# Kernel tuning notes

Measured on AMD Instinct MI355X. Metric: run time of the kernel, lower is better.

Reference implementation:

```python
import jax, jax.numpy as jnp
import numpy as np

N = 50000      # nodes
E = 800000     # edges
IN_C = 128
HID = 96
OUT_C = 40
L = 8          # num_layers
ALPHA = 0.1
THETA = 0.5
DROPOUT = 0.5


def setup_inputs() -> dict:
    key = jax.random.key(0)
    ks = jax.random.split(key, 6)
    x = jax.random.normal(ks[0], (N, IN_C), dtype=jnp.float32)
    edge_index = jax.random.randint(ks[1], (2, E), 0, N, dtype=jnp.int64)
    proj_w = jax.random.normal(ks[2], (IN_C, HID), dtype=jnp.float32) / np.sqrt(IN_C)
    proj_b = jnp.zeros((HID,), dtype=jnp.float32)
    conv_ws = jax.random.normal(ks[3], (L, HID, HID), dtype=jnp.float32) / np.sqrt(HID)
    out_w = jax.random.normal(ks[4], (2 * HID, OUT_C), dtype=jnp.float32) / np.sqrt(2 * HID)
    out_b = jnp.zeros((OUT_C,), dtype=jnp.float32)
    return {"x": x, "edge_index": edge_index, "proj_w": proj_w, "proj_b": proj_b,
            "conv_ws": conv_ws, "out_w": out_w, "out_b": out_b}


def reference(x, edge_index, proj_w, proj_b, conv_ws, out_w, out_b):
    # --- GCN normalization with self loops (computed once, as GCN2Conv caches it) ---
    loops = jnp.arange(N, dtype=edge_index.dtype)
    src = jnp.concatenate([edge_index[0], loops])   # [E+N]
    dst = jnp.concatenate([edge_index[1], loops])
    deg = jax.ops.segment_sum(jnp.ones(E + N, dtype=x.dtype), dst, num_segments=N)
    dis = jax.lax.rsqrt(deg)                        # deg >= 1 due to self loops
    norm = dis[src] * dis[dst]                      # [E+N]

    h0 = x @ proj_w + proj_b                        # [N, HID]
    h = h0
    key = jax.random.key(42)
    for k in range(L):
        delta = 1.0 / 2 ** k
        kq, ke, kd, key = jax.random.split(key, 4)
        # dithered quantization
        b = (jax.random.uniform(kq, h.shape, dtype=h.dtype) - 0.5) * delta
        h_q = jnp.floor((h + b) / delta) * delta - b
        # GCN2Conv: propagate + initial residual + identity mapping (shared weights)
        agg = jax.ops.segment_sum(h_q[src] * norm[:, None], dst, num_segments=N)
        t = (1.0 - ALPHA) * agg + ALPHA * h0
        beta = float(np.log(THETA / (k + 1) + 1.0))
        h = (1.0 - beta) * t + beta * (t @ conv_ws[k])
        # gaussian noise + relu
        h = jax.nn.relu(h + 0.01 * jax.random.normal(ke, h.shape, dtype=h.dtype))
        if k != L - 1:
            keep = 1.0 - DROPOUT
            mask = jax.random.bernoulli(kd, keep, h.shape)
            h = jnp.where(mask, h / keep, 0.0)
    return jnp.concatenate([h0, h], axis=-1) @ out_w + out_b
```

## Files before the change

kernel.cpp:

```cpp
#include <hip/hip_runtime.h>
#include <hip/hip_fp16.h>
#include <cstdint>
#include <cmath>

#define HID 96
#define INC 128
#define OUTC 40
#define ROWS 32

__device__ __forceinline__ unsigned rotl32d(unsigned x, int r){ return (x<<r)|(x>>(32-r)); }

__device__ __forceinline__ void tf2x32_dev(unsigned k0, unsigned k1, unsigned x0, unsigned x1,
                                           unsigned &y0, unsigned &y1){
  unsigned ks2 = k0 ^ k1 ^ 0x1BD11BDAu;
  x0 += k0; x1 += k1;
#define TFR(r) { x0 += x1; x1 = rotl32d(x1, r); x1 ^= x0; }
  TFR(13) TFR(15) TFR(26) TFR(6)   x0 += k1;  x1 += ks2 + 1u;
  TFR(17) TFR(29) TFR(16) TFR(24)  x0 += ks2; x1 += k0 + 2u;
  TFR(13) TFR(15) TFR(26) TFR(6)   x0 += k0;  x1 += k1 + 3u;
  TFR(17) TFR(29) TFR(16) TFR(24)  x0 += k1;  x1 += ks2 + 4u;
  TFR(13) TFR(15) TFR(26) TFR(6)   x0 += ks2; x1 += k0 + 5u;
#undef TFR
  y0 = x0; y1 = x1;
}

__device__ __forceinline__ unsigned tf_bits(unsigned k0, unsigned k1, unsigned idx){
  unsigned y0, y1; tf2x32_dev(k0, k1, 0u, idx, y0, y1); return y0 ^ y1;
}

__device__ __forceinline__ float u01_from_bits(unsigned bits){
  return __uint_as_float((bits >> 9) | 0x3f800000u) - 1.0f;
}

__device__ __forceinline__ float erfinv_xla(float x){
  float w = -log1pf(-x*x);
  float p;
  if (w < 5.0f){
    w = w - 2.5f;
    p = 2.81022636e-08f;
    p = fmaf(p,w, 3.43273939e-07f);
    p = fmaf(p,w,-3.5233877e-06f);
    p = fmaf(p,w,-4.39150654e-06f);
    p = fmaf(p,w, 0.00021858087f);
    p = fmaf(p,w,-0.00125372503f);
    p = fmaf(p,w,-0.00417768164f);
    p = fmaf(p,w, 0.246640727f);
    p = fmaf(p,w, 1.50140941f);
  } else {
    w = sqrtf(w) - 3.0f;
    p = -0.000200214257f;
    p = fmaf(p,w, 0.000100950558f);
    p = fmaf(p,w, 0.00134934322f);
    p = fmaf(p,w,-0.00367342844f);
    p = fmaf(p,w, 0.00573950773f);
    p = fmaf(p,w,-0.0076224613f);
    p = fmaf(p,w, 0.00943887047f);
    p = fmaf(p,w, 1.00167406f);
    p = fmaf(p,w, 2.83297682f);
  }
  return p*x;
}

__global__ void k_detect(const unsigned* __restrict__ raw, int* flag){
  unsigned v = raw[2*threadIdx.x + 1];
  unsigned long long m = __ballot(v == 0u);
  if (threadIdx.x == 0) *flag = (m == 0xFFFFFFFFFFFFFFFFull) ? 1 : 0;
}

__global__ void k_convcount(const unsigned* __restrict__ raw, const int* __restrict__ flag,
                            int E, int* __restrict__ cnt){
  int e = blockIdx.x*256 + threadIdx.x; if (e >= E) return;
  int d;
  if (*flag) d = (int)raw[2*((size_t)E + e)];
  else       d = ((const int*)raw)[E + e];
  atomicAdd(&cnt[d], 1);
}

__global__ void k_psum_histo(const int* __restrict__ cnt, int N,
                             int* __restrict__ psum, int* __restrict__ bcnt){
  __shared__ int sh[256];
  __shared__ int lh[64];
  int tid = threadIdx.x; int n = blockIdx.x*256 + tid;
  int v = (n < N) ? cnt[n] : 0;
  int vp = (v + 7) & ~7;
  sh[tid] = vp;
  if (tid < 64) lh[tid] = 0;
  __syncthreads();
  if (n < N) atomicAdd(&lh[min(v, 63)], 1);
  for (int off = 128; off > 0; off >>= 1){
    __syncthreads();
    if (tid < off) sh[tid] += sh[tid + off];
  }
  __syncthreads();
  if (tid == 0) psum[blockIdx.x] = sh[0];
  if (tid < 64){
    int c = lh[tid];
    if (c > 0) atomicAdd(&bcnt[tid], c);
  }
}

__global__ void k_scan2(int* __restrict__ psum, int nb, int* __restrict__ bcnt){
  __shared__ int sh[256];
  __shared__ int sb[64];
  int tid = threadIdx.x;
  int v = (tid < nb) ? psum[tid] : 0;
  sh[tid] = v;
  if (tid < 64) sb[tid] = bcnt[tid];
  __syncthreads();
  for (int off = 1; off < 256; off <<= 1){
    int t = (tid >= off) ? sh[tid - off] : 0;
    __syncthreads();
    sh[tid] += t;
    __syncthreads();
  }
  if (tid < nb) psum[tid] = sh[tid] - v;
  if (tid < 64){
    int off = 0;
    for (int b2 = tid+1; b2 < 64; b2++) off += sb[b2];
    bcnt[tid] = off;
  }
}

__global__ void k_rowptr_perm(const int* __restrict__ cnt, const int* __restrict__ psum,
                              int N, int* __restrict__ rowptr, float* __restrict__ dis,
                              int* __restrict__ bcnt, int* __restrict__ perm,
                              int* __restrict__ csr_src, float* __restrict__ csr_w){
  __shared__ int sh[256];
  __shared__ int lh[64];
  int tid = threadIdx.x; int n = blockIdx.x*256 + tid;
  int v = (n < N) ? cnt[n] : 0;
  int vp = (v + 7) & ~7;
  sh[tid] = vp;
  if (tid < 64) lh[tid] = 0;
  __syncthreads();
  int b = min(v, 63), r = 0;
  if (n < N) r = atomicAdd(&lh[b], 1);
  for (int off = 1; off < 256; off <<= 1){
    int t = (tid >= off) ? sh[tid - off] : 0;
    __syncthreads();
    sh[tid] += t;
    __syncthreads();
  }
  if (n < N){
    int rp = psum[blockIdx.x] + sh[tid] - vp;
    rowptr[n] = rp;
    dis[n] = 1.0f / sqrtf((float)(v + 1));
    for (int q = v; q < vp; q++){ csr_src[rp + q] = 0; csr_w[rp + q] = 0.0f; }
    if (n == N-1) rowptr[N] = rp + vp;
  }
  if (tid < 64){
    int c = lh[tid];
    lh[tid] = (c > 0) ? atomicAdd(&bcnt[tid], c) : 0;
  }
  __syncthreads();
  if (n < N) perm[lh[b] + r] = n;
}

__global__ void k_fill(const unsigned* __restrict__ raw, const int* __restrict__ flag, int E,
                       const int* __restrict__ rowptr, int* __restrict__ cnt,
                       const float* __restrict__ dis,
                       int* __restrict__ csr_src, float* __restrict__ csr_w){
  int e = blockIdx.x*256 + threadIdx.x; if (e >= E) return;
  int s, d;
  if (*flag){ s = (int)raw[2*(size_t)e]; d = (int)raw[2*((size_t)E + e)]; }
  else      { const int* r = (const int*)raw; s = r[e]; d = r[E + e]; }
  int pos = atomicAdd(&cnt[d], 1);
  int slot = rowptr[d] + pos;
  csr_src[slot] = s;
  csr_w[slot] = dis[s]*dis[d];
}

__global__ __launch_bounds__(256) void k_h0(
  const float* __restrict__ x, const float* __restrict__ W, const float* __restrict__ bias,
  float* __restrict__ h0, __half* __restrict__ hq, unsigned kq0, unsigned kq1, int N)
{
  __shared__ float xs[64*65];
  __shared__ float wsh[64*96];
  int tid = threadIdx.x; int n0 = blockIdx.x*64;
  int cg = tid & 15, ng = tid >> 4; int c0 = cg*6;
  float acc[4][6];
#pragma unroll
  for (int i=0;i<4;i++) for (int j=0;j<6;j++) acc[i][j]=0.f;
  for (int kc=0; kc<2; kc++){
    if (kc) __syncthreads();
    for (int q=tid; q<1536; q+=256)
      ((float4*)wsh)[q] = ((const float4*)(W + kc*64*96))[q];
    for (int q=tid; q<1024; q+=256){
      int g=q*4; int r=g>>6, col=g&63;
      int n=n0+r; int ns = n<N ? n : N-1;
      float4 v = ((const float4*)(x + (size_t)ns*128 + kc*64))[col>>2];
      xs[r*65+col]=v.x; xs[r*65+col+1]=v.y; xs[r*65+col+2]=v.z; xs[r*65+col+3]=v.w;
    }
    __syncthreads();
    for (int k=0;k<64;k++){
      float wv[6];
#pragma unroll
      for (int j=0;j<6;j++) wv[j]=wsh[k*96 + c0 + j];
#pragma unroll
      for (int i=0;i<4;i++){
        float xv = xs[(ng*4+i)*65 + k];
#pragma unroll
        for (int j=0;j<6;j++) acc[i][j] = fmaf(xv, wv[j], acc[i][j]);
      }
    }
  }
#pragma unroll
  for (int i=0;i<4;i++){
    int n = n0 + ng*4 + i; if (n >= N) continue;
#pragma unroll
    for (int j=0;j<6;j++){
      int c = c0 + j; int p = n*96 + c;
      float v = acc[i][j] + bias[c];
      h0[p] = v;
      unsigned bq = tf_bits(kq0, kq1, (unsigned)p);
      float b = u01_from_bits(bq) - 0.5f;
      hq[(size_t)n*96 + c] = __float2half_rn(floorf(v + b) - b);
    }
  }
}

#define GATH(gj, wv) { \
  float2 f01 = __half22float2(*(__half2*)&gj.x); \
  float2 f23 = __half22float2(*(__half2*)&gj.y); \
  ax = fmaf(f01.x, wv, ax); ay = fmaf(f01.y, wv, ay); \
  az = fmaf(f23.x, wv, az); aw = fmaf(f23.y, wv, aw); }

__global__ __launch_bounds__(256, 6) void k_layer(
  const __half* __restrict__ hq_in, const float* __restrict__ h0, const float* __restrict__ dis,
  const int* __restrict__ rowptr, const int* __restrict__ csr_src, const float* __restrict__ csr_w,
  const int* __restrict__ perm, const float* __restrict__ W,
  float betaf, float ombf,
  unsigned ke0, unsigned ke1, unsigned kd0, unsigned kd1,
  unsigned kq0, unsigned kq1, float delta_n, float invdelta_n,
  int do_dropout, int write_h,
  __half* __restrict__ hq_out, float* __restrict__ h_out, int N)
{
  __shared__ float ts[ROWS*100];
  __shared__ float wsh[24*96];
  __shared__ int rowmap[ROWS];
  int tid = threadIdx.x;
  int tx = tid & 31, ty = tid >> 5;
  int n0 = blockIdx.x*ROWS;

  const char* hqc = (const char*)hq_in;
  const char* h0c = (const char*)h0;

#pragma unroll 1
  for (int pass = 0; pass < 4; pass++){
    int r = pass*8 + ty;
    int row = n0 + r;
    int n = (row < N) ? perm[row] : -1;
    if (tx == 0) rowmap[r] = n;
    if (tx < 24){
      float4 o = make_float4(0.f, 0.f, 0.f, 0.f);
      if (n >= 0){
        float d = dis[n];
        unsigned lo = (unsigned)rowptr[n], hi = (unsigned)rowptr[n+1];
        unsigned txb = (unsigned)tx*8u;
        uint2 sraw = *(const uint2*)(hqc + (unsigned)n*192u + txb);
        float2 s01 = __half22float2(*(__half2*)&sraw.x);
        float2 s23 = __half22float2(*(__half2*)&sraw.y);
        float dd = d*d;
        float ax = s01.x*dd, ay = s01.y*dd, az = s23.x*dd, aw = s23.y*dd;
        for (unsigned s = lo; s < hi; s += 8){
          int4   sa = *(const int4*)(csr_src + s);
          int4   sb = *(const int4*)(csr_src + s + 4);
          float4 wa = *(const float4*)(csr_w + s);
          float4 wb = *(const float4*)(csr_w + s + 4);
          uint2 g0 = *(const uint2*)(hqc + (unsigned)sa.x*192u + txb);
          uint2 g1 = *(const uint2*)(hqc + (unsigned)sa.y*192u + txb);
          uint2 g2 = *(const uint2*)(hqc + (unsigned)sa.z*192u + txb);
          uint2 g3 = *(const uint2*)(hqc + (unsigned)sa.w*192u + txb);
          uint2 g4 = *(const uint2*)(hqc + (unsigned)sb.x*192u + txb);
          uint2 g5 = *(const uint2*)(hqc + (unsigned)sb.y*192u + txb);
          uint2 g6 = *(const uint2*)(hqc + (unsigned)sb.z*192u + txb);
          uint2 g7 = *(const uint2*)(hqc + (unsigned)sb.w*192u + txb);
          GATH(g0, wa.x) GATH(g1, wa.y) GATH(g2, wa.z) GATH(g3, wa.w)
          GATH(g4, wb.x) GATH(g5, wb.y) GATH(g6, wb.z) GATH(g7, wb.w)
        }
        float4 hz = *(const float4*)(h0c + (unsigned)n*384u + (unsigned)tx*16u);
        o.x = 0.9f*ax + 0.1f*hz.x;
        o.y = 0.9f*ay + 0.1f*hz.y;
        o.z = 0.9f*az + 0.1f*hz.z;
        o.w = 0.9f*aw + 0.1f*hz.w;
      }
      *((float4*)&ts[r*100 + tx*4]) = o;
    }
  }

  int cg = tid & 7, ng = tid >> 3;
  int c0 = cg * 12;
  float acc[12];
#pragma unroll
  for (int j = 0; j < 12; j++) acc[j] = 0.f;

  for (int chunk = 0; chunk < 4; chunk++){
    __syncthreads();
    for (int q = tid; q < 576; q += 256)
      ((float4*)wsh)[q] = ((const float4*)(W + chunk*24*96))[q];
    __syncthreads();
#pragma unroll 4
    for (int kk = 0; kk < 24; kk++){
      int k = chunk*24 + kk;
      float4 w0 = *((const float4*)&wsh[kk*96 + c0]);
      float4 w1 = *((const float4*)&wsh[kk*96 + c0 + 4]);
      float4 w2 = *((const float4*)&wsh[kk*96 + c0 + 8]);
      float xv = ts[ng*100 + k];
      acc[0] = fmaf(xv, w0.x, acc[0]);  acc[1] = fmaf(xv, w0.y, acc[1]);
      acc[2] = fmaf(xv, w0.z, acc[2]);  acc[3] = fmaf(xv, w0.w, acc[3]);
      acc[4] = fmaf(xv, w1.x, acc[4]);  acc[5] = fmaf(xv, w1.y, acc[5]);
      acc[6] = fmaf(xv, w1.z, acc[6]);  acc[7] = fmaf(xv, w1.w, acc[7]);
      acc[8] = fmaf(xv, w2.x, acc[8]);  acc[9] = fmaf(xv, w2.y, acc[9]);
      acc[10]= fmaf(xv, w2.z, acc[10]); acc[11]= fmaf(xv, w2.w, acc[11]);
    }
  }

  const float LO = __uint_as_float(0xBF7FFFFFu);
  int n = rowmap[ng];
  if (n >= 0){
    float res[12];
#pragma unroll
    for (int j = 0; j < 12; j++){
      int c = c0 + j; unsigned p = (unsigned)n*96u + (unsigned)c;
      float tv = ts[ng*100 + c];
      float hv = ombf*tv + betaf*acc[j];
      unsigned be = tf_bits(ke0, ke1, p);
      float uv = fmaxf(LO, u01_from_bits(be)*2.0f + LO);
      hv += 0.01f * (1.41421356f * erfinv_xla(uv));
      hv = fmaxf(hv, 0.0f);
      if (do_dropout){
        unsigned bd = tf_bits(kd0, kd1, p);
        hv = (bd < 0x80000000u) ? hv*2.0f : 0.0f;
      }
      if (!write_h){
        unsigned bq = tf_bits(kq0, kq1, p);
        float b = (u01_from_bits(bq) - 0.5f)*delta_n;
        hv = floorf((hv + b)*invdelta_n)*delta_n - b;
      }
      res[j] = hv;
    }
    if (write_h){
      float* dst2 = h_out + (size_t)n*96 + c0;
#pragma unroll
      for (int j4 = 0; j4 < 3; j4++)
        *((float4*)&dst2[j4*4]) = make_float4(res[j4*4], res[j4*4+1], res[j4*4+2], res[j4*4+3]);
    } else {
      uint2* dst2 = (uint2*)(hq_out + (size_t)n*96 + c0);
#pragma unroll
      for (int j4 = 0; j4 < 3; j4++){
        unsigned lo2 = (unsigned)__half_as_ushort(__float2half_rn(res[j4*4+0]))
                     | ((unsigned)__half_as_ushort(__float2half_rn(res[j4*4+1])) << 16);
        unsigned hi2 = (unsigned)__half_as_ushort(__float2half_rn(res[j4*4+2]))
                     | ((unsigned)__half_as_ushort(__float2half_rn(res[j4*4+3])) << 16);
        dst2[j4] = make_uint2(lo2, hi2);
      }
    }
  }
}

__global__ __launch_bounds__(256) void k_final(
  const float* __restrict__ h0, const float* __restrict__ h,
  const float* __restrict__ W, const float* __restrict__ bias,
  float* __restrict__ out, int N)
{
  __shared__ float xs[64*97];
  __shared__ float wsh[96*40];
  int tid = threadIdx.x; int n0 = blockIdx.x*64;
  int cg = tid & 7, ng = tid >> 3; int c0 = cg*5;
  float acc[2][5];
#pragma unroll
  for (int i=0;i<2;i++) for (int j=0;j<5;j++) acc[i][j]=0.f;
  for (int ph=0; ph<2; ph++){
    if (ph) __syncthreads();
    const float* xsrc = ph ? h : h0;
    for (int q=tid; q<960; q+=256)
      ((float4*)wsh)[q] = ((const float4*)(W + ph*96*40))[q];
    for (int q=tid; q<1536; q+=256){
      int g=q*4; int r=g/96, col=g%96;
      int n=n0+r; int ns = n<N ? n : N-1;
      float4 v = ((const float4*)(xsrc + (size_t)ns*96))[col>>2];
      xs[r*97+col]=v.x; xs[r*97+col+1]=v.y; xs[r*97+col+2]=v.z; xs[r*97+col+3]=v.w;
    }
    __syncthreads();
    for (int k=0;k<96;k++){
      float wv[5];
#pragma unroll
      for (int j=0;j<5;j++) wv[j]=wsh[k*40 + c0 + j];
#pragma unroll
      for (int i=0;i<2;i++){
        float xv = xs[(ng*2+i)*97 + k];
#pragma unroll
        for (int j=0;j<5;j++) acc[i][j] = fmaf(xv, wv[j], acc[i][j]);
      }
    }
  }
#pragma unroll
  for (int i=0;i<2;i++){
    int n = n0 + ng*2 + i; if (n >= N) continue;
#pragma unroll
    for (int j=0;j<5;j++)
      out[(size_t)n*40 + c0 + j] = acc[i][j] + bias[c0 + j];
  }
}

static void tf_host(uint32_t k0, uint32_t k1, uint32_t x0, uint32_t x1,
                    uint32_t &y0, uint32_t &y1){
  uint32_t ks2 = k0 ^ k1 ^ 0x1BD11BDAu;
  x0 += k0; x1 += k1;
  auto R = [&](int r){ x0 += x1; x1 = (x1<<r)|(x1>>(32-r)); x1 ^= x0; };
  R(13);R(15);R(26);R(6);   x0 += k1;  x1 += ks2 + 1u;
  R(17);R(29);R(16);R(24);  x0 += ks2; x1 += k0 + 2u;
  R(13);R(15);R(26);R(6);   x0 += k0;  x1 += k1 + 3u;
  R(17);R(29);R(16);R(24);  x0 += k1;  x1 += ks2 + 4u;
  R(13);R(15);R(26);R(6);   x0 += ks2; x1 += k0 + 5u;
  y0 = x0; y1 = x1;
}

extern "C" void kernel_launch(void* const* d_in, const int* in_sizes, int n_in,
                              void* d_out, int out_size, void* d_ws, size_t ws_size,
                              hipStream_t stream)
{
  const float*    x       = (const float*)d_in[0];
  const unsigned* eraw    = (const unsigned*)d_in[1];
  const float*    proj_w  = (const float*)d_in[2];
  const float*    proj_b  = (const float*)d_in[3];
  const float*    conv_w  = (const float*)d_in[4];
  const float*    out_w   = (const float*)d_in[5];
  const float*    out_b   = (const float*)d_in[6];
  float* out = (float*)d_out;

  const int N = in_sizes[0] / INC;
  const int E = in_sizes[1] / 2;
  const size_t NH = (size_t)N * HID;
  const int EP = ((E + 7*N + 15) & ~15);

  float*  ws     = (float*)d_ws;
  float*  h0     = ws;
  __half* hqA    = (__half*)(h0 + NH);
  __half* hqB    = hqA + NH;
  float*  hb     = (float*)(hqB + NH);
  float*  dis    = hb + NH;
  int*    cnt    = (int*)(dis + N);
  int*    rowptr = cnt + N;
  int*    csr_src= rowptr + ((N + 16) & ~15);
  float*  csr_w  = (float*)(csr_src + EP);
  int*    flag   = (int*)(csr_w + EP);
  int*    perm   = flag + 16;
  int*    bcnt   = perm + ((N + 15) & ~15);
  int*    psum   = bcnt + 64;
  (void)ws_size; (void)n_in; (void)out_size;

  uint32_t kq[8][2], ke[8][2], kd[8][2];
  {
    uint32_t K0 = 0u, K1 = 42u;
    for (int k = 0; k < 8; k++){
      uint32_t y0, y1;
      tf_host(K0, K1, 0u, 0u, y0, y1); kq[k][0]=y0; kq[k][1]=y1;
      tf_host(K0, K1, 0u, 1u, y0, y1); ke[k][0]=y0; ke[k][1]=y1;
      tf_host(K0, K1, 0u, 2u, y0, y1); kd[k][0]=y0; kd[k][1]=y1;
      tf_host(K0, K1, 0u, 3u, y0, y1); K0=y0; K1=y1;
    }
  }

  const int gE  = (E + 255)/256;
  const int gN  = (N + 255)/256;
  const int gMM = (N + 63)/64;
  const int gL  = (N + ROWS-1)/ROWS;

  hipMemsetAsync(cnt, 0, (size_t)N*4, stream);
  hipMemsetAsync(bcnt, 0, 64*4, stream);
  k_detect <<<1, 64, 0, stream>>>(eraw, flag);
  k_convcount<<<gE, 256, 0, stream>>>(eraw, flag, E, cnt);
  k_psum_histo<<<gN, 256, 0, stream>>>(cnt, N, psum, bcnt);
  k_scan2  <<<1, 256, 0, stream>>>(psum, gN, bcnt);
  k_rowptr_perm<<<gN, 256, 0, stream>>>(cnt, psum, N, rowptr, dis, bcnt, perm, csr_src, csr_w);
  hipMemsetAsync(cnt, 0, (size_t)N*4, stream);
  k_fill   <<<gE, 256, 0, stream>>>(eraw, flag, E, rowptr, cnt, dis, csr_src, csr_w);

  k_h0<<<gMM, 256, 0, stream>>>(x, proj_w, proj_b, h0, hqA, kq[0][0], kq[0][1], N);

  for (int k = 0; k < 8; k++){
    double bd = log(0.5/(double)(k+1) + 1.0);
    float betaf = (float)bd;
    float ombf  = (float)(1.0 - bd);
    int last = (k == 7);
    float dn  = 1.0f/(float)(1 << (k+1));
    float idn = (float)(1 << (k+1));
    const __half* hin  = (k & 1) ? hqB : hqA;
    __half*       hout = (k & 1) ? hqA : hqB;
    k_layer<<<gL, 256, 0, stream>>>(hin, h0, dis, rowptr, csr_src, csr_w, perm,
      conv_w + (size_t)k*HID*HID, betaf, ombf,
      ke[k][0], ke[k][1], kd[k][0], kd[k][1],
      last?0u:kq[k+1][0], last?0u:kq[k+1][1], dn, idn,
      !last, last, hout, hb, N);
  }

  k_final<<<gMM, 256, 0, stream>>>(h0, hb, out_w, out_b, out, N);
}
```

Before: 977.1 us.

## Renumber nodes into degree-sorted order so layer kernel works on contiguous rows

Node features, h0, normalization and CSR are all stored in a permuted, degree-bucketed index space, so each layer block reads contiguous rowptr/h0/hq rows instead of indirecting through perm. The inverse permutation is applied once in CSR fill, h0 projection and final output. The gather loop is also unrolled to 16 edges, and non-temporal loads/stores are used for the streaming CSR and output data, with launch bounds occupancy lowered from 6 to 4. The cost is extra preprocessing kernels and scattered writes in setup. Gathers from neighbours stay random in the new order.

```diff
diff --git a/kernel.cpp b/kernel.cpp
--- a/kernel.cpp
+++ b/kernel.cpp
@@ -7,6 +7,27 @@
 #define INC 128
 #define OUTC 40
 #define ROWS 32
+
+typedef int      v4i __attribute__((ext_vector_type(4)));
+typedef float    v4f __attribute__((ext_vector_type(4)));
+typedef unsigned v2u __attribute__((ext_vector_type(2)));
+
+__device__ __forceinline__ int4 ntld_i4(const int* p){
+  v4i v = __builtin_nontemporal_load((const v4i*)p);
+  return make_int4(v.x, v.y, v.z, v.w);
+}
+__device__ __forceinline__ float4 ntld_f4(const float* p){
+  v4f v = __builtin_nontemporal_load((const v4f*)p);
+  return make_float4(v.x, v.y, v.z, v.w);
+}
+__device__ __forceinline__ void ntst_u2(void* p, unsigned lo, unsigned hi){
+  v2u v; v.x = lo; v.y = hi;
+  __builtin_nontemporal_store(v, (v2u*)p);
+}
+__device__ __forceinline__ void ntst_f4(float* p, float a, float b, float c, float d){
+  v4f v; v.x = a; v.y = b; v.z = c; v.w = d;
+  __builtin_nontemporal_store(v, (v4f*)p);
+}
 
 __device__ __forceinline__ unsigned rotl32d(unsigned x, int r){ return (x<<r)|(x>>(32-r)); }
 
@@ -76,36 +97,74 @@
   atomicAdd(&cnt[d], 1);
 }
 
-__global__ void k_psum_histo(const int* __restrict__ cnt, int N,
-                             int* __restrict__ psum, int* __restrict__ bcnt){
-  __shared__ int sh[256];
+__global__ void k_hist(const int* __restrict__ cnt, int N, int* __restrict__ bcnt){
+  __shared__ int lh[64];
+  int tid = threadIdx.x; int n = blockIdx.x*256 + tid;
+  if (tid < 64) lh[tid] = 0;
+  __syncthreads();
+  if (n < N) atomicAdd(&lh[min(cnt[n], 63)], 1);
+  __syncthreads();
+  if (tid < 64){
+    int c = lh[tid];
+    if (c > 0) atomicAdd(&bcnt[tid], c);
+  }
+}
+
+__global__ void k_bucketoff(int* __restrict__ bcnt){
+  __shared__ int sb[64];
+  int tid = threadIdx.x;
+  sb[tid] = bcnt[tid];
+  __syncthreads();
+  int off = 0;
+  for (int b2 = tid+1; b2 < 64; b2++) off += sb[b2];
+  bcnt[tid] = off;
+}
+
+__global__ void k_perm(const int* __restrict__ cnt, int N, int* __restrict__ boff,
+                       int* __restrict__ perm, int* __restrict__ iperm,
+                       float* __restrict__ diso, float* __restrict__ dsqr,
+                       int* __restrict__ degv, int* __restrict__ degp){
   __shared__ int lh[64];
   int tid = threadIdx.x; int n = blockIdx.x*256 + tid;
   int v = (n < N) ? cnt[n] : 0;
-  int vp = (v + 7) & ~7;
-  sh[tid] = vp;
   if (tid < 64) lh[tid] = 0;
   __syncthreads();
-  if (n < N) atomicAdd(&lh[min(v, 63)], 1);
-  for (int off = 128; off > 0; off >>= 1){
-    __syncthreads();
-    if (tid < off) sh[tid] += sh[tid + off];
-  }
-  __syncthreads();
-  if (tid == 0) psum[blockIdx.x] = sh[0];
+  int b = min(v, 63), r = 0;
+  if (n < N) r = atomicAdd(&lh[b], 1);
+  __syncthreads();
   if (tid < 64){
     int c = lh[tid];
-    if (c > 0) atomicAdd(&bcnt[tid], c);
-  }
-}
-
-__global__ void k_scan2(int* __restrict__ psum, int nb, int* __restrict__ bcnt){
+    lh[tid] = (c > 0) ? atomicAdd(&boff[tid], c) : 0;
+  }
+  __syncthreads();
+  if (n < N){
+    int pos = lh[b] + r;
+    perm[pos] = n;
+    iperm[n] = pos;
+    diso[n] = 1.0f / sqrtf((float)(v + 1));
+    dsqr[pos] = 1.0f / (float)(v + 1);
+    degv[pos] = v;
+    degp[pos] = (v + 7) & ~7;
+  }
+}
+
+__global__ void k_scanA(const int* __restrict__ degp, int N, int* __restrict__ psum){
   __shared__ int sh[256];
-  __shared__ int sb[64];
+  int tid = threadIdx.x; int n = blockIdx.x*256 + tid;
+  sh[tid] = (n < N) ? degp[n] : 0;
+  for (int off = 128; off > 0; off >>= 1){
+    __syncthreads();
+    if (tid < off) sh[tid] += sh[tid + off];
+  }
+  __syncthreads();
+  if (tid == 0) psum[blockIdx.x] = sh[0];
+}
+
+__global__ void k_scanB(int* __restrict__ psum, int nb){
+  __shared__ int sh[256];
   int tid = threadIdx.x;
   int v = (tid < nb) ? psum[tid] : 0;
   sh[tid] = v;
-  if (tid < 64) sb[tid] = bcnt[tid];
   __syncthreads();
   for (int off = 1; off < 256; off <<= 1){
     int t = (tid >= off) ? sh[tid - off] : 0;
@@ -114,27 +173,17 @@
     __syncthreads();
   }
   if (tid < nb) psum[tid] = sh[tid] - v;
-  if (tid < 64){
-    int off = 0;
-    for (int b2 = tid+1; b2 < 64; b2++) off += sb[b2];
-    bcnt[tid] = off;
-  }
-}
-
-__global__ void k_rowptr_perm(const int* __restrict__ cnt, const int* __restrict__ psum,
-                              int N, int* __restrict__ rowptr, float* __restrict__ dis,
-                              int* __restrict__ bcnt, int* __restrict__ perm,
-                              int* __restrict__ csr_src, float* __restrict__ csr_w){
+}
+
+__global__ void k_rowptr2(const int* __restrict__ degv, const int* __restrict__ degp,
+                          const int* __restrict__ psum, int N,
+                          int* __restrict__ rowptr, int* __restrict__ csr_src,
+                          float* __restrict__ csr_w){
   __shared__ int sh[256];
-  __shared__ int lh[64];
   int tid = threadIdx.x; int n = blockIdx.x*256 + tid;
-  int v = (n < N) ? cnt[n] : 0;
-  int vp = (v + 7) & ~7;
+  int vp = (n < N) ? degp[n] : 0;
   sh[tid] = vp;
-  if (tid < 64) lh[tid] = 0;
-  __syncthreads();
-  int b = min(v, 63), r = 0;
-  if (n < N) r = atomicAdd(&lh[b], 1);
+  __syncthreads();
   for (int off = 1; off < 256; off <<= 1){
     int t = (tid >= off) ? sh[tid - off] : 0;
     __syncthreads();
@@ -142,37 +191,33 @@
     __syncthreads();
   }
   if (n < N){
-    int rp = psum[blockIdx.x] + sh[tid] - vp;
-    rowptr[n] = rp;
-    dis[n] = 1.0f / sqrtf((float)(v + 1));
-    for (int q = v; q < vp; q++){ csr_src[rp + q] = 0; csr_w[rp + q] = 0.0f; }
-    if (n == N-1) rowptr[N] = rp + vp;
-  }
-  if (tid < 64){
-    int c = lh[tid];
-    lh[tid] = (c > 0) ? atomicAdd(&bcnt[tid], c) : 0;
-  }
-  __syncthreads();
-  if (n < N) perm[lh[b] + r] = n;
+    int base = psum[blockIdx.x] + sh[tid] - vp;
+    rowptr[n] = base;
+    int v = degv[n];
+    for (int q = v; q < vp; q++){ csr_src[base + q] = 0; csr_w[base + q] = 0.0f; }
+    if (n == N-1) rowptr[N] = base + vp;
+  }
 }
 
 __global__ void k_fill(const unsigned* __restrict__ raw, const int* __restrict__ flag, int E,
-                       const int* __restrict__ rowptr, int* __restrict__ cnt,
-                       const float* __restrict__ dis,
+                       const int* __restrict__ rowptr, const int* __restrict__ iperm,
+                       int* __restrict__ cur, const float* __restrict__ diso,
                        int* __restrict__ csr_src, float* __restrict__ csr_w){
   int e = blockIdx.x*256 + threadIdx.x; if (e >= E) return;
   int s, d;
   if (*flag){ s = (int)raw[2*(size_t)e]; d = (int)raw[2*((size_t)E + e)]; }
   else      { const int* r = (const int*)raw; s = r[e]; d = r[E + e]; }
-  int pos = atomicAdd(&cnt[d], 1);
-  int slot = rowptr[d] + pos;
-  csr_src[slot] = s;
-  csr_w[slot] = dis[s]*dis[d];
+  int rd = iperm[d];
+  int pos = atomicAdd(&cur[rd], 1);
+  int slot = rowptr[rd] + pos;
+  csr_src[slot] = iperm[s];
+  csr_w[slot] = diso[s]*diso[d];
 }
 
 __global__ __launch_bounds__(256) void k_h0(
   const float* __restrict__ x, const float* __restrict__ W, const float* __restrict__ bias,
-  float* __restrict__ h0, __half* __restrict__ hq, unsigned kq0, unsigned kq1, int N)
+  const int* __restrict__ iperm,
+  float* __restrict__ h0p, __half* __restrict__ hq, unsigned kq0, unsigned kq1, int N)
 {
   __shared__ float xs[64*65];
   __shared__ float wsh[64*96];
@@ -207,14 +252,15 @@
 #pragma unroll
   for (int i=0;i<4;i++){
     int n = n0 + ng*4 + i; if (n >= N) continue;
+    int rn = iperm[n];
 #pragma unroll
     for (int j=0;j<6;j++){
       int c = c0 + j; int p = n*96 + c;
       float v = acc[i][j] + bias[c];
-      h0[p] = v;
+      h0p[(size_t)rn*96 + c] = v;
       unsigned bq = tf_bits(kq0, kq1, (unsigned)p);
       float b = u01_from_bits(bq) - 0.5f;
-      hq[(size_t)n*96 + c] = __float2half_rn(floorf(v + b) - b);
+      hq[(size_t)rn*96 + c] = __float2half_rn(floorf(v + b) - b);
     }
   }
 }
@@ -225,8 +271,8 @@
   ax = fmaf(f01.x, wv, ax); ay = fmaf(f01.y, wv, ay); \
   az = fmaf(f23.x, wv, az); aw = fmaf(f23.y, wv, aw); }
 
-__global__ __launch_bounds__(256, 6) void k_layer(
-  const __half* __restrict__ hq_in, const float* __restrict__ h0, const float* __restrict__ dis,
+__global__ __launch_bounds__(256, 4) void k_layer(
+  const __half* __restrict__ hq_in, const float* __restrict__ h0p, const float* __restrict__ dsqr,
   const int* __restrict__ rowptr, const int* __restrict__ csr_src, const float* __restrict__ csr_w,
   const int* __restrict__ perm, const float* __restrict__ W,
   float betaf, float ombf,
@@ -237,36 +283,64 @@
 {
   __shared__ float ts[ROWS*100];
   __shared__ float wsh[24*96];
-  __shared__ int rowmap[ROWS];
   int tid = threadIdx.x;
   int tx = tid & 31, ty = tid >> 5;
   int n0 = blockIdx.x*ROWS;
 
   const char* hqc = (const char*)hq_in;
-  const char* h0c = (const char*)h0;
 
 #pragma unroll 1
   for (int pass = 0; pass < 4; pass++){
     int r = pass*8 + ty;
     int row = n0 + r;
-    int n = (row < N) ? perm[row] : -1;
-    if (tx == 0) rowmap[r] = n;
     if (tx < 24){
       float4 o = make_float4(0.f, 0.f, 0.f, 0.f);
-      if (n >= 0){
-        float d = dis[n];
-        unsigned lo = (unsigned)rowptr[n], hi = (unsigned)rowptr[n+1];
+      if (row < N){
         unsigned txb = (unsigned)tx*8u;
-        uint2 sraw = *(const uint2*)(hqc + (unsigned)n*192u + txb);
+        float dd = dsqr[row];
+        unsigned lo = (unsigned)rowptr[row], hi = (unsigned)rowptr[row+1];
+        uint2 sraw = *(const uint2*)(hqc + (unsigned)row*192u + txb);
+        float4 hz = ntld_f4(h0p + (size_t)row*96 + tx*4);
         float2 s01 = __half22float2(*(__half2*)&sraw.x);
         float2 s23 = __half22float2(*(__half2*)&sraw.y);
-        float dd = d*d;
         float ax = s01.x*dd, ay = s01.y*dd, az = s23.x*dd, aw = s23.y*dd;
-        for (unsigned s = lo; s < hi; s += 8){
-          int4   sa = *(const int4*)(csr_src + s);
-          int4   sb = *(const int4*)(csr_src + s + 4);
-          float4 wa = *(const float4*)(csr_w + s);
-          float4 wb = *(const float4*)(csr_w + s + 4);
+        unsigned s = lo;
+        unsigned n16 = lo + ((hi - lo) & ~15u);
+        for (; s < n16; s += 16){
+          int4   sa = ntld_i4(csr_src + s);
+          int4   sb = ntld_i4(csr_src + s + 4);
+          int4   sc = ntld_i4(csr_src + s + 8);
+          int4   sd = ntld_i4(csr_src + s + 12);
+          float4 wa = ntld_f4(csr_w + s);
+          float4 wb = ntld_f4(csr_w + s + 4);
+          float4 wc = ntld_f4(csr_w + s + 8);
+          float4 wd = ntld_f4(csr_w + s + 12);
+          uint2 g0 = *(const uint2*)(hqc + (unsigned)sa.x*192u + txb);
+          uint2 g1 = *(const uint2*)(hqc + (unsigned)sa.y*192u + txb);
+          uint2 g2 = *(const uint2*)(hqc + (unsigned)sa.z*192u + txb);
+          uint2 g3 = *(const uint2*)(hqc + (unsigned)sa.w*192u + txb);
+          uint2 g4 = *(const uint2*)(hqc + (unsigned)sb.x*192u + txb);
+          uint2 g5 = *(const uint2*)(hqc + (unsigned)sb.y*192u + txb);
+          uint2 g6 = *(const uint2*)(hqc + (unsigned)sb.z*192u + txb);
+          uint2 g7 = *(const uint2*)(hqc + (unsigned)sb.w*192u + txb);
+          uint2 g8 = *(const uint2*)(hqc + (unsigned)sc.x*192u + txb);
+          uint2 g9 = *(const uint2*)(hqc + (unsigned)sc.y*192u + txb);
+          uint2 gA = *(const uint2*)(hqc + (unsigned)sc.z*192u + txb);
+          uint2 gB = *(const uint2*)(hqc + (unsigned)sc.w*192u + txb);
+          uint2 gC = *(const uint2*)(hqc + (unsigned)sd.x*192u + txb);
+          uint2 gD = *(const uint2*)(hqc + (unsigned)sd.y*192u + txb);
+          uint2 gE = *(const uint2*)(hqc + (unsigned)sd.z*192u + txb);
+          uint2 gF = *(const uint2*)(hqc + (unsigned)sd.w*192u + txb);
+          GATH(g0, wa.x) GATH(g1, wa.y) GATH(g2, wa.z) GATH(g3, wa.w)
+          GATH(g4, wb.x) GATH(g5, wb.y) GATH(g6, wb.z) GATH(g7, wb.w)
+          GATH(g8, wc.x) GATH(g9, wc.y) GATH(gA, wc.z) GATH(gB, wc.w)
+          GATH(gC, wd.x) GATH(gD, wd.y) GATH(gE, wd.z) GATH(gF, wd.w)
+        }
+        for (; s < hi; s += 8){
+          int4   sa = ntld_i4(csr_src + s);
+          int4   sb = ntld_i4(csr_src + s + 4);
+          float4 wa = ntld_f4(csr_w + s);
+          float4 wb = ntld_f4(csr_w + s + 4);
           uint2 g0 = *(const uint2*)(hqc + (unsigned)sa.x*192u + txb);
           uint2 g1 = *(const uint2*)(hqc + (unsigned)sa.y*192u + txb);
           uint2 g2 = *(const uint2*)(hqc + (unsigned)sa.z*192u + txb);
@@ -278,7 +352,6 @@
           GATH(g0, wa.x) GATH(g1, wa.y) GATH(g2, wa.z) GATH(g3, wa.w)
           GATH(g4, wb.x) GATH(g5, wb.y) GATH(g6, wb.z) GATH(g7, wb.w)
         }
-        float4 hz = *(const float4*)(h0c + (unsigned)n*384u + (unsigned)tx*16u);
         o.x = 0.9f*ax + 0.1f*hz.x;
         o.y = 0.9f*ay + 0.1f*hz.y;
         o.z = 0.9f*az + 0.1f*hz.z;
@@ -316,12 +389,13 @@
   }
 
   const float LO = __uint_as_float(0xBF7FFFFFu);
-  int n = rowmap[ng];
-  if (n >= 0){
+  int n = n0 + ng;
+  if (n < N){
+    int po = perm[n];
     float res[12];
 #pragma unroll
     for (int j = 0; j < 12; j++){
-      int c = c0 + j; unsigned p = (unsigned)n*96u + (unsigned)c;
+      int c = c0 + j; unsigned p = (unsigned)po*96u + (unsigned)c;
       float tv = ts[ng*100 + c];
       float hv = ombf*tv + betaf*acc[j];
       unsigned be = tf_bits(ke0, ke1, p);
@@ -343,25 +417,25 @@
       float* dst2 = h_out + (size_t)n*96 + c0;
 #pragma unroll
       for (int j4 = 0; j4 < 3; j4++)
-        *((float4*)&dst2[j4*4]) = make_float4(res[j4*4], res[j4*4+1], res[j4*4+2], res[j4*4+3]);
+        ntst_f4(&dst2[j4*4], res[j4*4], res[j4*4+1], res[j4*4+2], res[j4*4+3]);
     } else {
-      uint2* dst2 = (uint2*)(hq_out + (size_t)n*96 + c0);
+      __half* dst2 = hq_out + (size_t)n*96 + c0;
 #pragma unroll
       for (int j4 = 0; j4 < 3; j4++){
         unsigned lo2 = (unsigned)__half_as_ushort(__float2half_rn(res[j4*4+0]))
                      | ((unsigned)__half_as_ushort(__float2half_rn(res[j4*4+1])) << 16);
         unsigned hi2 = (unsigned)__half_as_ushort(__float2half_rn(res[j4*4+2]))
                      | ((unsigned)__half_as_ushort(__float2half_rn(res[j4*4+3])) << 16);
-        dst2[j4] = make_uint2(lo2, hi2);
+        ntst_u2(dst2 + j4*4, lo2, hi2);
       }
     }
   }
 }
 
 __global__ __launch_bounds__(256) void k_final(
-  const float* __restrict__ h0, const float* __restrict__ h,
+  const float* __restrict__ h0p, const float* __restrict__ hp,
   const float* __restrict__ W, const float* __restrict__ bias,
-  float* __restrict__ out, int N)
+  const int* __restrict__ perm, float* __restrict__ out, int N)
 {
   __shared__ float xs[64*97];
   __shared__ float wsh[96*40];
@@ -372,7 +446,7 @@
   for (int i=0;i<2;i++) for (int j=0;j<5;j++) acc[i][j]=0.f;
   for (int ph=0; ph<2; ph++){
     if (ph) __syncthreads();
-    const float* xsrc = ph ? h : h0;
+    const float* xsrc = ph ? hp : h0p;
     for (int q=tid; q<960; q+=256)
       ((float4*)wsh)[q] = ((const float4*)(W + ph*96*40))[q];
     for (int q=tid; q<1536; q+=256){
@@ -397,9 +471,10 @@
 #pragma unroll
   for (int i=0;i<2;i++){
     int n = n0 + ng*2 + i; if (n >= N) continue;
+    int pm = perm[n];
 #pragma unroll
     for (int j=0;j<5;j++)
-      out[(size_t)n*40 + c0 + j] = acc[i][j] + bias[c0 + j];
+      out[(size_t)pm*40 + c0 + j] = acc[i][j] + bias[c0 + j];
   }
 }
 
@@ -432,22 +507,28 @@
   const int N = in_sizes[0] / INC;
   const int E = in_sizes[1] / 2;
   const size_t NH = (size_t)N * HID;
+  const int NP = (N + 16) & ~15;
   const int EP = ((E + 7*N + 15) & ~15);
 
   float*  ws     = (float*)d_ws;
-  float*  h0     = ws;
-  __half* hqA    = (__half*)(h0 + NH);
+  float*  h0p    = ws;
+  float*  hbp    = h0p + NH;
+  __half* hqA    = (__half*)(hbp + NH);
   __half* hqB    = hqA + NH;
-  float*  hb     = (float*)(hqB + NH);
-  float*  dis    = hb + NH;
-  int*    cnt    = (int*)(dis + N);
-  int*    rowptr = cnt + N;
-  int*    csr_src= rowptr + ((N + 16) & ~15);
-  float*  csr_w  = (float*)(csr_src + EP);
-  int*    flag   = (int*)(csr_w + EP);
-  int*    perm   = flag + 16;
-  int*    bcnt   = perm + ((N + 15) & ~15);
+  float*  csr_w  = (float*)(hqB + NH);
+  int*    csr_src= (int*)(csr_w + EP);
+  int*    rowptr = csr_src + EP;
+  int*    perm   = rowptr + NP;
+  int*    iperm  = perm + NP;
+  int*    degv   = iperm + NP;
+  int*    degp   = degv + NP;
+  int*    cnt    = degp + NP;
+  int*    cur    = cnt + NP;
+  float*  diso   = (float*)(cur + NP);
+  float*  dsqr   = diso + NP;
+  int*    bcnt   = (int*)(dsqr + NP);
   int*    psum   = bcnt + 64;
+  int*    flag   = psum + 256;
   (void)ws_size; (void)n_in; (void)out_size;
 
   uint32_t kq[8][2], ke[8][2], kd[8][2];
@@ -469,15 +550,18 @@
 
   hipMemsetAsync(cnt, 0, (size_t)N*4, stream);
   hipMemsetAsync(bcnt, 0, 64*4, stream);
-  k_detect <<<1, 64, 0, stream>>>(eraw, flag);
+  k_detect   <<<1, 64, 0, stream>>>(eraw, flag);
   k_convcount<<<gE, 256, 0, stream>>>(eraw, flag, E, cnt);
-  k_psum_histo<<<gN, 256, 0, stream>>>(cnt, N, psum, bcnt);
-  k_scan2  <<<1, 256, 0, stream>>>(psum, gN, bcnt);
-  k_rowptr_perm<<<gN, 256, 0, stream>>>(cnt, psum, N, rowptr, dis, bcnt, perm, csr_src, csr_w);
-  hipMemsetAsync(cnt, 0, (size_t)N*4, stream);
-  k_fill   <<<gE, 256, 0, stream>>>(eraw, flag, E, rowptr, cnt, dis, csr_src, csr_w);
-
-  k_h0<<<gMM, 256, 0, stream>>>(x, proj_w, proj_b, h0, hqA, kq[0][0], kq[0][1], N);
+  k_hist     <<<gN, 256, 0, stream>>>(cnt, N, bcnt);
+  k_bucketoff<<<1, 64, 0, stream>>>(bcnt);
+  k_perm     <<<gN, 256, 0, stream>>>(cnt, N, bcnt, perm, iperm, diso, dsqr, degv, degp);
+  k_scanA    <<<gN, 256, 0, stream>>>(degp, N, psum);
+  k_scanB    <<<1, 256, 0, stream>>>(psum, gN);
+  k_rowptr2  <<<gN, 256, 0, stream>>>(degv, degp, psum, N, rowptr, csr_src, csr_w);
+  hipMemsetAsync(cur, 0, (size_t)N*4, stream);
+  k_fill     <<<gE, 256, 0, stream>>>(eraw, flag, E, rowptr, iperm, cur, diso, csr_src, csr_w);
+
+  k_h0<<<gMM, 256, 0, stream>>>(x, proj_w, proj_b, iperm, h0p, hqA, kq[0][0], kq[0][1], N);
 
   for (int k = 0; k < 8; k++){
     double bd = log(0.5/(double)(k+1) + 1.0);
@@ -488,12 +572,12 @@
     float idn = (float)(1 << (k+1));
     const __half* hin  = (k & 1) ? hqB : hqA;
     __half*       hout = (k & 1) ? hqA : hqB;
-    k_layer<<<gL, 256, 0, stream>>>(hin, h0, dis, rowptr, csr_src, csr_w, perm,
+    k_layer<<<gL, 256, 0, stream>>>(hin, h0p, dsqr, rowptr, csr_src, csr_w, perm,
       conv_w + (size_t)k*HID*HID, betaf, ombf,
       ke[k][0], ke[k][1], kd[k][0], kd[k][1],
       last?0u:kq[k+1][0], last?0u:kq[k+1][1], dn, idn,
-      !last, last, hout, hb, N);
-  }
-
-  k_final<<<gMM, 256, 0, stream>>>(h0, hb, out_w, out_b, out, N);
-}
+      !last, last, hout, hbp, N);
+  }
+
+  k_final<<<gMM, 256, 0, stream>>>(h0p, hbp, out_w, out_b, perm, out, N);
+}
```

After: 983.8 us. No clear change (+0.7%).
